# Kernel optimization log

Measured on AMD Instinct MI355X. Metric: run time of the kernel, lower is better.

The kernel has to match this reference:

```python
import jax, jax.numpy as jnp
import numpy as np

ALPHA, BETA, GAMMA = 1.0, 1.0, 0.7
WIN = 11
C1 = 0.01 ** 2
C2 = 0.03 ** 2


def get_sobel_kernels(n1=1, n2=2, n3=2):
    a = np.asarray
    Sx = a([[[-n1, 0, n1], [-n2, 0, n2], [-n1, 0, n1]],
            [[-n2, 0, n2], [-n3 * n2, 0, n3 * n2], [-n2, 0, n2]],
            [[-n1, 0, n1], [-n2, 0, n2], [-n1, 0, n1]]])
    Sy = a([[[-n1, -n2, -n1], [0, 0, 0], [n1, n2, n1]],
            [[-n2, -n3 * n2, -n2], [0, 0, 0], [n2, n3 * n2, n2]],
            [[-n1, -n2, -n1], [0, 0, 0], [n1, n2, n1]]])
    Sz = a([[[-n1, -n2, -n1], [-n2, -n3 * n2, -n2], [-n1, -n2, -n1]],
            [[0, 0, 0], [0, 0, 0], [0, 0, 0]],
            [[n1, n2, n1], [n2, n3 * n2, n2], [n1, n2, n1]]])
    Sd11 = a([[[0, n1, n2], [-n1, 0, n1], [-n2, -n1, 0]],
              [[0, n2, n2 * n3], [-n2, 0, n2], [-n2 * n3, -n2, 0]],
              [[0, n1, n2], [-n1, 0, n1], [-n2, -n1, 0]]])
    Sd12 = a([[[-n2, -n1, 0], [-n1, 0, n1], [0, n1, n2]],
              [[-n2 * n3, -n2, 0], [-n2, 0, n2], [0, n2, n2 * n3]],
              [[-n2, -n1, 0], [-n1, 0, n1], [0, n1, n2]]])
    Sd21 = Sd11.T
    Sd22 = Sd12.T
    Sd31 = a([-S.T for S in Sd11.T])
    Sd32 = a([S.T for S in Sd12.T])
    return np.stack([Sx, Sy, Sz, Sd11, Sd12, Sd21, Sd22, Sd31, Sd32]).astype(np.float32)

# (9,1,3,3,3) fused sobel bank -- single grouped conv instead of 9 launches
SOBEL_W = jnp.asarray(get_sobel_kernels()[:, None])


def _gauss1d():
    g = jnp.exp(-(jnp.arange(WIN, dtype=jnp.float32) - WIN // 2) ** 2 / (2 * 1.5 ** 2))
    return g / g.sum()

G1D = _gauss1d()


def conv3d(x, w):
    return jax.lax.conv_general_dilated(
        x, w, window_strides=(1, 1, 1), padding='SAME',
        dimension_numbers=('NCDHW', 'OIDHW', 'NCDHW'))


def gauss_filter(x):
    # separable 11-tap gaussian along D, H, W (== full 11^3 window, zero-padded SAME)
    x = conv3d(x, G1D.reshape(1, 1, WIN, 1, 1))
    x = conv3d(x, G1D.reshape(1, 1, 1, WIN, 1))
    x = conv3d(x, G1D.reshape(1, 1, 1, 1, WIN))
    return x


def edge_map(img):
    # GradEdge3D.__call__ with a=1, C=1
    B, C, D, H, W = img.shape
    xp = jnp.pad(img, ((0, 0), (0, 0), (1, 1), (1, 1), (1, 1)), mode='reflect')
    g = conv3d(xp, SOBEL_W)                       # (B, 9, D+2, H+2, W+2)
    gm = jnp.sqrt(jnp.sum((g + 1e-6) ** 2 + 1e-6, axis=1))  # (B, D+2, H+2, W+2)
    gm = gm[:, 1:-1, 1:-1, 1:-1]
    norm = (gm - gm.min()) / (gm.max() - gm.min() + 1e-6)
    return norm.reshape(B, 1, D, H, W)


def ssim_value(pred, target):
    mu_p = gauss_filter(pred)
    mu_t = gauss_filter(target)
    mu_p2, mu_t2, mu_pt = mu_p ** 2, mu_t ** 2, mu_p * mu_t
    sig_p = gauss_filter(pred * pred) - mu_p2
    sig_t = gauss_filter(target * target) - mu_t2
    sig_pt = gauss_filter(pred * target) - mu_pt
    ssim_map = ((2 * mu_pt + C1) * (2 * sig_pt + C2)) / ((mu_p2 + mu_t2 + C1) * (sig_p + sig_t + C2))
    return 1.0 - ssim_map.mean()


def setup_inputs() -> dict:
    key = jax.random.key(0)
    k1, k2 = jax.random.split(key)
    shape = (2, 1, 128, 128, 128)
    return {
        'pred': jax.random.uniform(k1, shape, dtype=jnp.float32),
        'target': jax.random.uniform(k2, shape, dtype=jnp.float32),
    }


def reference(pred, target):
    loss_mse = jnp.mean((pred - target) ** 2)
    loss_ssim = ssim_value(pred, target)
    # GMELoss3D: lam_errors=[(1.0, L1Loss())], reduction='sum'
    loss_gme = 1e-6 + jnp.mean(jnp.abs(edge_map(pred) - edge_map(target)))
    total = ALPHA * loss_mse + BETA * loss_ssim + GAMMA * loss_gme
    return (total, loss_mse, loss_ssim, loss_gme)
```

## Files before the change

kernel.cpp:

```cpp
#include <hip/hip_runtime.h>


#define VOL 4194304
#define HV  2097152

typedef _Float16 h2 __attribute__((ext_vector_type(2)));
typedef _Float16 h8 __attribute__((ext_vector_type(8)));

constexpr float GW[11] = {
    0.00102838f, 0.00759876f, 0.03600077f, 0.10936070f, 0.21300554f,
    0.26601173f,
    0.21300554f, 0.10936070f, 0.03600077f, 0.00759876f, 0.00102838f};


__global__ __launch_bounds__(256) void k_init(double* dbl, unsigned int* ui) {
  const int tid = threadIdx.x + (blockIdx.x << 8);
  if (tid < 1536) dbl[tid] = 0.0;
  if (tid < 4096) ui[tid] = (tid < 2048) ? 0x7F800000u : 0u;
}

__device__ __forceinline__ void wblur_body(
    const float* __restrict__ p, const float* __restrict__ t,
    _Float16* __restrict__ A, double* __restrict__ mseB, const int bidx) {
  __shared__ float pr[2][138];
  __shared__ float tr[2][138];
  __shared__ float redw[256];
  const int tid = threadIdx.x;
  const int rl = tid >> 7;
  const int x  = tid & 127;
  const int rowBase = bidx << 4;
  if (x < 5)    { pr[rl][x] = 0.f;      tr[rl][x] = 0.f; }
  if (x >= 123) { pr[rl][10 + x] = 0.f; tr[rl][10 + x] = 0.f; }
  float pv = p[((rowBase + rl) << 7) + x];
  float tv = t[((rowBase + rl) << 7) + x];
  float msel = 0.f;
  for (int it = 0; it < 8; ++it) {
    const int row  = rowBase + (it << 1) + rl;
    const int base = row << 7;
    pr[rl][5 + x] = pv; tr[rl][5 + x] = tv;
    __syncthreads();
    float pvN = 0.f, tvN = 0.f;
    if (it < 7) {
      const int baseN = (row + 2) << 7;
      pvN = p[baseN + x]; tvN = t[baseN + x];
    }
    float ap = 0.f, at = 0.f, app = 0.f, att = 0.f, apt = 0.f;
#pragma unroll
    for (int k = 0; k < 11; ++k) {
      const float w = GW[k];
      const float a = pr[rl][x + k];
      const float b = tr[rl][x + k];
      ap += w * a; at += w * b;
      app += w * a * a; att += w * b * b; apt += w * a * b;
    }
    const int idx = base + x;
    A[idx]           = (_Float16)ap;
    A[VOL + idx]     = (_Float16)at;
    A[2 * VOL + idx] = (_Float16)app;
    A[3 * VOL + idx] = (_Float16)att;
    A[4 * VOL + idx] = (_Float16)apt;
    const float d = pv - tv;
    msel += d * d;
    __syncthreads();
    pv = pvN; tv = tvN;
  }
  redw[tid] = msel;
  __syncthreads();
  for (int s = 128; s > 0; s >>= 1) {
    if (tid < s) redw[tid] += redw[tid + s];
    __syncthreads();
  }
  if (tid == 0) atomicAdd(&mseB[(bidx & 63) << 3], (double)redw[0]);
}

__device__ __forceinline__ void sobel_body(
    const float* __restrict__ p, const float* __restrict__ t,
    _Float16* __restrict__ gmP, _Float16* __restrict__ gmT,
    unsigned int* __restrict__ ui, const int bx, const int by, const int bz) {
  __shared__ float sb[972];
  __shared__ float rmin[256];
  __shared__ float rmax[256];
  const int tid = threadIdx.x;
  const int tx = tid & 15;
  const int ty = tid >> 4;
  const int x0 = bx << 4;
  const int y0 = by << 4;
  const int vol = bz >> 3;
  const int b   = (bz >> 2) & 1;
  const int z0  = (bz & 3) << 5;
  const float* __restrict__ img = vol ? t : p;
  _Float16* __restrict__ gm = vol ? gmT : gmP;
  const int vb = b << 21;

  const int l1 = tid;
  const int ly1 = l1 / 18, lx1 = l1 % 18;
  int gy1 = y0 - 1 + ly1; gy1 = gy1 < 0 ? 1 : (gy1 > 127 ? 126 : gy1);
  int gx1 = x0 - 1 + lx1; gx1 = gx1 < 0 ? 1 : (gx1 > 127 ? 126 : gx1);
  const int off1 = (gy1 << 7) + gx1;
  const int l2 = tid + 256;
  const int ly2 = l2 / 18, lx2 = l2 % 18;
  int gy2 = y0 - 1 + ly2; gy2 = gy2 < 0 ? 1 : (gy2 > 127 ? 126 : gy2);
  int gx2 = x0 - 1 + lx2; gx2 = gx2 < 0 ? 1 : (gx2 > 127 ? 126 : gx2);
  const int off2 = (gy2 << 7) + gx2;
  const bool has2 = (tid < 68);
  const int rb = ty * 18 + tx;
  const int gbase = vb + (z0 << 14) + ((y0 + ty) << 7) + (x0 + tx);

  float Y0[7], Y1[7], Y2[7];
  float rv1 = 0.f, rv2 = 0.f;
  float lmin = 3.4e38f, lmax = 0.f;

#define LOADR(ZS) {                                                         \
    const int zc_ = (ZS) > 127 ? 126 : (ZS);                                \
    const int za_ = vb + (zc_ << 14);                                       \
    rv1 = img[za_ + off1];                                                  \
    if (has2) rv2 = img[za_ + off2]; }

#define WRITELDS(BOFF) {                                                    \
    sb[(BOFF) + l1] = rv1;                                                  \
    if (has2) sb[(BOFF) + l2] = rv2; }

#define COMPY(P) {                                                          \
    const int o_ = (P) * 324 + rb;                                          \
    const float r00 = sb[o_],      r01 = sb[o_ + 1],  r02 = sb[o_ + 2];     \
    const float r10 = sb[o_ + 18], r11 = sb[o_ + 19], r12 = sb[o_ + 20];    \
    const float r20 = sb[o_ + 36], r21 = sb[o_ + 37], r22 = sb[o_ + 38];    \
    const float dx0 = r02 - r00, dx1 = r12 - r10, dx2 = r22 - r20;          \
    const float ux0 = r00 + r01 + r02, ux1 = r10 + r11 + r12,               \
                ux2 = r20 + r21 + r22;                                      \
    const float sx0 = ux0 + r01, sx1 = ux1 + r11, sx2 = ux2 + r21;          \
    Y##P[1] = dx0 + dx1 + dx2;                                    \
    Y##P[0] = Y##P[1] + dx1;                                      \
    Y##P[2] = sx2 - sx0;                                          \
    Y##P[4] = sx0 + sx1 + sx2;                                    \
    Y##P[3] = Y##P[4] + sx1;                                      \
    Y##P[5] = ux2 - ux0;                                          \
    Y##P[6] = (ux0 + ux2) + 2.f * ux1; }

#define EMIT(I, P0, P1, P2) {                                               \
    const float E_ = Y##P0[0] + Y##P1[0] + Y##P2[0];                        \
    const float g1 = E_ + Y##P1[0];                                         \
    const float tA = Y##P0[1] + Y##P1[1] + Y##P2[1];                        \
    const float A_ = tA + Y##P1[1];                                         \
    const float D_ = Y##P0[2] + Y##P1[2] + Y##P2[2];                        \
    const float g2 = D_ + Y##P1[2];                                         \
    const float g3 = Y##P2[3] - Y##P0[3];                                   \
    const float C_ = Y##P2[4] - Y##P0[4];                                   \
    const float B_ = (Y##P0[5] + Y##P2[5]) + 2.f * Y##P1[5];                \
    const float F_ = Y##P2[6] - Y##P0[6];                                   \
    const float g4 = A_ - B_, g5 = A_ + B_;                                 \
    const float g6 = C_ - D_, g7 = C_ + D_;                                 \
    const float g8 = E_ - F_, g9 = E_ + F_;                                 \
    float ss_ = 9e-6f, t_;                                                  \
    t_ = g1 + 1e-6f; ss_ = fmaf(t_, t_, ss_);                               \
    t_ = g2 + 1e-6f; ss_ = fmaf(t_, t_, ss_);                               \
    t_ = g3 + 1e-6f; ss_ = fmaf(t_, t_, ss_);                               \
    t_ = g4 + 1e-6f; ss_ = fmaf(t_, t_, ss_);                               \
    t_ = g5 + 1e-6f; ss_ = fmaf(t_, t_, ss_);                               \
    t_ = g6 + 1e-6f; ss_ = fmaf(t_, t_, ss_);                               \
    t_ = g7 + 1e-6f; ss_ = fmaf(t_, t_, ss_);                               \
    t_ = g8 + 1e-6f; ss_ = fmaf(t_, t_, ss_);                               \
    t_ = g9 + 1e-6f; ss_ = fmaf(t_, t_, ss_);                               \
    const _Float16 gh = (_Float16)sqrtf(ss_);                               \
    gm[gbase + ((I) << 14)] = gh;                                           \
    const float gq = (float)gh;                                             \
    lmin = fminf(lmin, gq); lmax = fmaxf(lmax, gq); }

#define BODY(I, P0, P1, P2) {                                               \
    WRITELDS((P2) * 324);                                                   \
    LOADR(z0 + (I) + 2);                                                    \
    __syncthreads();                                                        \
    COMPY(P2);                                                              \
    EMIT(I, P0, P1, P2); }

  {
    const int zp = (z0 == 0) ? 1 : (z0 - 1);
    LOADR(zp);  WRITELDS(0);
    LOADR(z0);  WRITELDS(324);
    __syncthreads();
    COMPY(0);
    COMPY(1);
    LOADR(z0 + 1);
  }
  for (int ii = 0; ii < 30; ii += 3) {
    BODY(ii,     0, 1, 2);
    BODY(ii + 1, 1, 2, 0);
    BODY(ii + 2, 2, 0, 1);
  }
  BODY(30, 0, 1, 2);
  BODY(31, 1, 2, 0);

#undef BODY
#undef EMIT
#undef COMPY
#undef WRITELDS
#undef LOADR

  rmin[tid] = lmin; rmax[tid] = lmax;
  __syncthreads();
  for (int st = 128; st > 0; st >>= 1) {
    if (tid < st) {
      rmin[tid] = fminf(rmin[tid], rmin[tid + st]);
      rmax[tid] = fmaxf(rmax[tid], rmax[tid + st]);
    }
    __syncthreads();
  }
  if (tid == 0) {
    const int bin = (bx + (by << 3) + (bz << 6)) & 63;
    atomicMin(&ui[vol * 1024 + (bin << 4)], __float_as_uint(rmin[0]));
    atomicMax(&ui[2048 + vol * 1024 + (bin << 4)], __float_as_uint(rmax[0]));
  }
}

__device__ __forceinline__ void blury_body(
    const _Float16* __restrict__ A, _Float16* __restrict__ B,
    const int z, const int yseg, const int batch) {
  __shared__ h8 s[5][26][16];
  const int tid = threadIdx.x;
  const int y0 = yseg << 4;
  const int b8 = batch << 18;
  const h8* __restrict__ Ah = (const h8*)A;
  h8* __restrict__ Bh = (h8*)B;
  const int slice8 = b8 + (z << 11);
  for (int q = 0; q < 5; ++q) {
    const h8* __restrict__ Aq = Ah + (q << 19) + slice8;
    for (int l = tid; l < 416; l += 256) {
      const int row = l >> 4, xc = l & 15;
      const int y = y0 - 5 + row;
      h8 v{};
      if ((unsigned)y < 128u) v = Aq[(y << 4) + xc];
      s[q][row][xc] = v;
    }
  }
  __syncthreads();
  const int xc = tid & 15;
  const int yo = tid >> 4;
  const int wbase = slice8 + ((y0 + yo) << 4) + xc;
#pragma unroll
  for (int q = 0; q < 5; ++q) {
    h8 acc{};
#pragma unroll
    for (int k = 0; k < 11; ++k) {
      const _Float16 w = (_Float16)GW[k];
      acc += w * s[q][yo + k][xc];
    }
    Bh[(q << 19) + wbase] = acc;
  }
}

__device__ __forceinline__ void edge_body(
    const _Float16* __restrict__ gmP, const _Float16* __restrict__ gmT,
    const unsigned int* __restrict__ ui, double* __restrict__ absB,
    const int bidx) {
  __shared__ float rede[256];
  float mnp = 3.4e38f, mnt = 3.4e38f, mxp = 0.f, mxt = 0.f;
  for (int j = 0; j < 64; ++j) {
    mnp = fminf(mnp, __uint_as_float(ui[j << 4]));
    mnt = fminf(mnt, __uint_as_float(ui[1024 + (j << 4)]));
    mxp = fmaxf(mxp, __uint_as_float(ui[2048 + (j << 4)]));
    mxt = fmaxf(mxt, __uint_as_float(ui[3072 + (j << 4)]));
  }
  const float scp = 1.f / (mxp - mnp + 1e-6f);
  const float sct = 1.f / (mxt - mnt + 1e-6f);
  const h8* __restrict__ gp = (const h8*)gmP;
  const h8* __restrict__ gt = (const h8*)gmT;
  float lsum = 0.f;
  const int base = bidx << 9;
#pragma unroll
  for (int i = 0; i < 2; ++i) {
    const int idx = base + (i << 8) + threadIdx.x;
    const h8 a = gp[idx];
    const h8 b = gt[idx];
#pragma unroll
    for (int j = 0; j < 8; ++j)
      lsum += fabsf(((float)a[j] - mnp) * scp - ((float)b[j] - mnt) * sct);
  }
  rede[threadIdx.x] = lsum;
  __syncthreads();
  for (int s = 128; s > 0; s >>= 1) {
    if (threadIdx.x < s) rede[threadIdx.x] += rede[threadIdx.x + s];
    __syncthreads();
  }
  if (threadIdx.x == 0)
    atomicAdd(&absB[(bidx & 63) << 3], (double)rede[0]);
}

__global__ __launch_bounds__(256) void k_fused_a(
    const float* __restrict__ p, const float* __restrict__ t,
    _Float16* __restrict__ A, double* __restrict__ mseB,
    _Float16* __restrict__ gmP, _Float16* __restrict__ gmT,
    unsigned int* __restrict__ ui) {
  const int bid = blockIdx.x;
  const int r3 = bid % 3;
  if (r3 < 2) {
    wblur_body(p, t, A, mseB, (bid / 3) * 2 + r3);
  } else {
    const int s = bid / 3;
    sobel_body(p, t, gmP, gmT, ui, s & 7, (s >> 3) & 7, s >> 6);
  }
}

__global__ __launch_bounds__(256) void k_fused_b(
    const _Float16* __restrict__ A, _Float16* __restrict__ B,
    const _Float16* __restrict__ gmP, const _Float16* __restrict__ gmT,
    const unsigned int* __restrict__ ui, double* __restrict__ absB) {
  const int bid = blockIdx.x;
  const int r3 = bid % 3;
  if (r3 < 2) {
    const int idx = (bid / 3) * 2 + r3;
    blury_body(A, B, idx & 127, (idx >> 7) & 7, idx >> 10);
  } else {
    edge_body(gmP, gmT, ui, absB, bid / 3);
  }
}

__global__ __launch_bounds__(256) void k_zblur_ssim(
    const _Float16* __restrict__ B, double* __restrict__ ssimB) {
  __shared__ h8 s[5][26][16];
  __shared__ float red[256];
  const int tid = threadIdx.x;
  const int y  = blockIdx.x;
  const int z0 = blockIdx.y << 4;
  const int b8 = blockIdx.z << 18;
  const h8* __restrict__ Bh = (const h8*)B;
  const int col8 = b8 + (y << 4);
  for (int q = 0; q < 5; ++q) {
    const h8* __restrict__ Bq = Bh + (q << 19) + col8;
    for (int l = tid; l < 416; l += 256) {
      const int row = l >> 4, xc = l & 15;
      const int zz = z0 - 5 + row;
      h8 v{};
      if ((unsigned)zz < 128u) v = Bq[(zz << 11) + xc];
      s[q][row][xc] = v;
    }
  }
  __syncthreads();
  const int xc = tid & 15;
  const int zo = tid >> 4;
  h8 m[5];
#pragma unroll
  for (int q = 0; q < 5; ++q) {
    h8 acc{};
#pragma unroll
    for (int k = 0; k < 11; ++k) {
      const _Float16 w = (_Float16)GW[k];
      acc += w * s[q][zo + k][xc];
    }
    m[q] = acc;
  }
  float lsum = 0.f;
#pragma unroll
  for (int j = 0; j < 8; ++j) {
    const float mp  = (float)m[0][j];
    const float mt  = (float)m[1][j];
    const float epp = (float)m[2][j];
    const float ett = (float)m[3][j];
    const float ept = (float)m[4][j];
    const float mp2 = mp * mp, mt2 = mt * mt, mpt = mp * mt;
    const float num = (2.f * mpt + 1e-4f) * (2.f * (ept - mpt) + 9e-4f);
    const float den = (mp2 + mt2 + 1e-4f) * ((epp - mp2) + (ett - mt2) + 9e-4f);
    lsum += num / den;
  }
  red[tid] = lsum;
  __syncthreads();
  for (int st = 128; st > 0; st >>= 1) {
    if (tid < st) red[tid] += red[tid + st];
    __syncthreads();
  }
  if (tid == 0) {
    const int bin = (blockIdx.x + (blockIdx.y << 3) + blockIdx.z) & 63;
    atomicAdd(&ssimB[bin << 3], (double)red[0]);
  }
}

__global__ void k_final(const double* __restrict__ dbl, float* __restrict__ out) {
  if (threadIdx.x == 0 && blockIdx.x == 0) {
    double ms = 0.0, ss = 0.0, ab = 0.0;
    for (int j = 0; j < 64; ++j) {
      ms += dbl[j << 3];
      ss += dbl[512 + (j << 3)];
      ab += dbl[1024 + (j << 3)];
    }
    const double N = 4194304.0;
    const double mse   = ms / N;
    const double ssiml = 1.0 - ss / N;
    const double gme   = 1e-6 + ab / N;
    const double total = mse + ssiml + 0.7 * gme;
    out[0] = (float)total;
    out[1] = (float)mse;
    out[2] = (float)ssiml;
    out[3] = (float)gme;
  }
}

extern "C" void kernel_launch(void* const* d_in, const int* in_sizes, int n_in,
                              void* d_out, int out_size, void* d_ws, size_t ws_size,
                              hipStream_t stream) {
  const float* p = (const float*)d_in[0];
  const float* t = (const float*)d_in[1];
  _Float16* A = (_Float16*)d_ws;
  _Float16* B = A + (size_t)5 * VOL;
  char* accb = (char*)d_ws + (size_t)20 * VOL;
  double* dbl = (double*)accb;
  unsigned int* ui = (unsigned int*)(accb + 12288);
  _Float16* gmP = (_Float16*)((char*)d_ws + 88080384);
  _Float16* gmT = gmP + VOL;
  float* out = (float*)d_out;

  k_init<<<16, 256, 0, stream>>>(dbl, ui);
  k_fused_a<<<3072, 256, 0, stream>>>(p, t, A, dbl, gmP, gmT, ui);
  k_fused_b<<<3072, 256, 0, stream>>>(A, B, gmP, gmT, ui, dbl + 1024);
  k_zblur_ssim<<<dim3(128, 8, 2), 256, 0, stream>>>(B, dbl + 512);
  k_final<<<1, 64, 0, stream>>>(dbl, out);
}
```

Measured before the change: 161.6 us.

## Blur sum/difference fields to cut SSIM channels from five to four

SSIM statistics are rebuilt from blurs of s=p+t and d=p-t and their squares instead of p, t, p², t², pt. This cuts the blurred fp16 channels from five to four, reducing memory traffic and arithmetic in all three blur passes. Separately, the Sobel LDS tile row stride is padded from 18 to 24 floats, likely to change bank mapping. The algebraic rewrite subtracts nearly equal fp16 quantities, so cancellation can cost some precision in the variance terms.

```diff
diff --git a/kernel.cpp b/kernel.cpp
--- a/kernel.cpp
+++ b/kernel.cpp
@@ -22,45 +22,47 @@
 __device__ __forceinline__ void wblur_body(
     const float* __restrict__ p, const float* __restrict__ t,
     _Float16* __restrict__ A, double* __restrict__ mseB, const int bidx) {
-  __shared__ float pr[2][138];
-  __shared__ float tr[2][138];
+  __shared__ float sr[2][138];
+  __shared__ float dr[2][138];
   __shared__ float redw[256];
   const int tid = threadIdx.x;
   const int rl = tid >> 7;
   const int x  = tid & 127;
   const int rowBase = bidx << 4;
-  if (x < 5)    { pr[rl][x] = 0.f;      tr[rl][x] = 0.f; }
-  if (x >= 123) { pr[rl][10 + x] = 0.f; tr[rl][10 + x] = 0.f; }
+  if (x < 5)    { sr[rl][x] = 0.f;      dr[rl][x] = 0.f; }
+  if (x >= 123) { sr[rl][10 + x] = 0.f; dr[rl][10 + x] = 0.f; }
   float pv = p[((rowBase + rl) << 7) + x];
   float tv = t[((rowBase + rl) << 7) + x];
   float msel = 0.f;
   for (int it = 0; it < 8; ++it) {
     const int row  = rowBase + (it << 1) + rl;
     const int base = row << 7;
-    pr[rl][5 + x] = pv; tr[rl][5 + x] = tv;
+    const float sv = pv + tv;
+    const float dv = pv - tv;
+    sr[rl][5 + x] = sv; dr[rl][5 + x] = dv;
+    msel += dv * dv;
     __syncthreads();
     float pvN = 0.f, tvN = 0.f;
     if (it < 7) {
       const int baseN = (row + 2) << 7;
       pvN = p[baseN + x]; tvN = t[baseN + x];
     }
-    float ap = 0.f, at = 0.f, app = 0.f, att = 0.f, apt = 0.f;
+    float as = 0.f, ad = 0.f, ass = 0.f, add_ = 0.f;
 #pragma unroll
     for (int k = 0; k < 11; ++k) {
       const float w = GW[k];
-      const float a = pr[rl][x + k];
-      const float b = tr[rl][x + k];
-      ap += w * a; at += w * b;
-      app += w * a * a; att += w * b * b; apt += w * a * b;
+      const float a = sr[rl][x + k];
+      const float b = dr[rl][x + k];
+      const float wa = w * a;
+      const float wb = w * b;
+      as += wa; ad += wb;
+      ass += wa * a; add_ += wb * b;
     }
     const int idx = base + x;
-    A[idx]           = (_Float16)ap;
-    A[VOL + idx]     = (_Float16)at;
-    A[2 * VOL + idx] = (_Float16)app;
-    A[3 * VOL + idx] = (_Float16)att;
-    A[4 * VOL + idx] = (_Float16)apt;
-    const float d = pv - tv;
-    msel += d * d;
+    A[idx]           = (_Float16)as;
+    A[VOL + idx]     = (_Float16)ad;
+    A[2 * VOL + idx] = (_Float16)ass;
+    A[3 * VOL + idx] = (_Float16)add_;
     __syncthreads();
     pv = pvN; tv = tvN;
   }
@@ -77,7 +79,7 @@
     const float* __restrict__ p, const float* __restrict__ t,
     _Float16* __restrict__ gmP, _Float16* __restrict__ gmT,
     unsigned int* __restrict__ ui, const int bx, const int by, const int bz) {
-  __shared__ float sb[972];
+  __shared__ float sb[1296];
   __shared__ float rmin[256];
   __shared__ float rmax[256];
   const int tid = threadIdx.x;
@@ -94,16 +96,18 @@
 
   const int l1 = tid;
   const int ly1 = l1 / 18, lx1 = l1 % 18;
+  const int la1 = ly1 * 24 + lx1;
   int gy1 = y0 - 1 + ly1; gy1 = gy1 < 0 ? 1 : (gy1 > 127 ? 126 : gy1);
   int gx1 = x0 - 1 + lx1; gx1 = gx1 < 0 ? 1 : (gx1 > 127 ? 126 : gx1);
   const int off1 = (gy1 << 7) + gx1;
   const int l2 = tid + 256;
   const int ly2 = l2 / 18, lx2 = l2 % 18;
+  const int la2 = ly2 * 24 + lx2;
   int gy2 = y0 - 1 + ly2; gy2 = gy2 < 0 ? 1 : (gy2 > 127 ? 126 : gy2);
   int gx2 = x0 - 1 + lx2; gx2 = gx2 < 0 ? 1 : (gx2 > 127 ? 126 : gx2);
   const int off2 = (gy2 << 7) + gx2;
   const bool has2 = (tid < 68);
-  const int rb = ty * 18 + tx;
+  const int rb = ty * 24 + tx;
   const int gbase = vb + (z0 << 14) + ((y0 + ty) << 7) + (x0 + tx);
 
   float Y0[7], Y1[7], Y2[7];
@@ -117,14 +121,14 @@
     if (has2) rv2 = img[za_ + off2]; }
 
 #define WRITELDS(BOFF) {                                                    \
-    sb[(BOFF) + l1] = rv1;                                                  \
-    if (has2) sb[(BOFF) + l2] = rv2; }
+    sb[(BOFF) + la1] = rv1;                                                 \
+    if (has2) sb[(BOFF) + la2] = rv2; }
 
 #define COMPY(P) {                                                          \
-    const int o_ = (P) * 324 + rb;                                          \
+    const int o_ = (P) * 432 + rb;                                          \
     const float r00 = sb[o_],      r01 = sb[o_ + 1],  r02 = sb[o_ + 2];     \
-    const float r10 = sb[o_ + 18], r11 = sb[o_ + 19], r12 = sb[o_ + 20];    \
-    const float r20 = sb[o_ + 36], r21 = sb[o_ + 37], r22 = sb[o_ + 38];    \
+    const float r10 = sb[o_ + 24], r11 = sb[o_ + 25], r12 = sb[o_ + 26];    \
+    const float r20 = sb[o_ + 48], r21 = sb[o_ + 49], r22 = sb[o_ + 50];    \
     const float dx0 = r02 - r00, dx1 = r12 - r10, dx2 = r22 - r20;          \
     const float ux0 = r00 + r01 + r02, ux1 = r10 + r11 + r12,               \
                 ux2 = r20 + r21 + r22;                                      \
@@ -167,7 +171,7 @@
     lmin = fminf(lmin, gq); lmax = fmaxf(lmax, gq); }
 
 #define BODY(I, P0, P1, P2) {                                               \
-    WRITELDS((P2) * 324);                                                   \
+    WRITELDS((P2) * 432);                                                   \
     LOADR(z0 + (I) + 2);                                                    \
     __syncthreads();                                                        \
     COMPY(P2);                                                              \
@@ -176,7 +180,7 @@
   {
     const int zp = (z0 == 0) ? 1 : (z0 - 1);
     LOADR(zp);  WRITELDS(0);
-    LOADR(z0);  WRITELDS(324);
+    LOADR(z0);  WRITELDS(432);
     __syncthreads();
     COMPY(0);
     COMPY(1);
@@ -215,14 +219,14 @@
 __device__ __forceinline__ void blury_body(
     const _Float16* __restrict__ A, _Float16* __restrict__ B,
     const int z, const int yseg, const int batch) {
-  __shared__ h8 s[5][26][16];
+  __shared__ h8 s[4][26][16];
   const int tid = threadIdx.x;
   const int y0 = yseg << 4;
   const int b8 = batch << 18;
   const h8* __restrict__ Ah = (const h8*)A;
   h8* __restrict__ Bh = (h8*)B;
   const int slice8 = b8 + (z << 11);
-  for (int q = 0; q < 5; ++q) {
+  for (int q = 0; q < 4; ++q) {
     const h8* __restrict__ Aq = Ah + (q << 19) + slice8;
     for (int l = tid; l < 416; l += 256) {
       const int row = l >> 4, xc = l & 15;
@@ -237,7 +241,7 @@
   const int yo = tid >> 4;
   const int wbase = slice8 + ((y0 + yo) << 4) + xc;
 #pragma unroll
-  for (int q = 0; q < 5; ++q) {
+  for (int q = 0; q < 4; ++q) {
     h8 acc{};
 #pragma unroll
     for (int k = 0; k < 11; ++k) {
@@ -316,7 +320,7 @@
 
 __global__ __launch_bounds__(256) void k_zblur_ssim(
     const _Float16* __restrict__ B, double* __restrict__ ssimB) {
-  __shared__ h8 s[5][26][16];
+  __shared__ h8 s[4][26][16];
   __shared__ float red[256];
   const int tid = threadIdx.x;
   const int y  = blockIdx.x;
@@ -324,7 +328,7 @@
   const int b8 = blockIdx.z << 18;
   const h8* __restrict__ Bh = (const h8*)B;
   const int col8 = b8 + (y << 4);
-  for (int q = 0; q < 5; ++q) {
+  for (int q = 0; q < 4; ++q) {
     const h8* __restrict__ Bq = Bh + (q << 19) + col8;
     for (int l = tid; l < 416; l += 256) {
       const int row = l >> 4, xc = l & 15;
@@ -337,9 +341,9 @@
   __syncthreads();
   const int xc = tid & 15;
   const int zo = tid >> 4;
-  h8 m[5];
-#pragma unroll
-  for (int q = 0; q < 5; ++q) {
+  h8 m[4];
+#pragma unroll
+  for (int q = 0; q < 4; ++q) {
     h8 acc{};
 #pragma unroll
     for (int k = 0; k < 11; ++k) {
@@ -351,14 +355,15 @@
   float lsum = 0.f;
 #pragma unroll
   for (int j = 0; j < 8; ++j) {
-    const float mp  = (float)m[0][j];
-    const float mt  = (float)m[1][j];
-    const float epp = (float)m[2][j];
-    const float ett = (float)m[3][j];
-    const float ept = (float)m[4][j];
-    const float mp2 = mp * mp, mt2 = mt * mt, mpt = mp * mt;
-    const float num = (2.f * mpt + 1e-4f) * (2.f * (ept - mpt) + 9e-4f);
-    const float den = (mp2 + mt2 + 1e-4f) * ((epp - mp2) + (ett - mt2) + 9e-4f);
+    const float mus = (float)m[0][j];
+    const float mud = (float)m[1][j];
+    const float ess = (float)m[2][j];
+    const float edd = (float)m[3][j];
+    const float S2 = mus * mus, D2 = mud * mud;
+    const float num = ((S2 - D2) * 0.5f + 1e-4f) *
+                      ((ess - edd - S2 + D2) * 0.5f + 9e-4f);
+    const float den = ((S2 + D2) * 0.5f + 1e-4f) *
+                      ((ess + edd - S2 - D2) * 0.5f + 9e-4f);
     lsum += num / den;
   }
   red[tid] = lsum;
@@ -399,7 +404,7 @@
   const float* p = (const float*)d_in[0];
   const float* t = (const float*)d_in[1];
   _Float16* A = (_Float16*)d_ws;
-  _Float16* B = A + (size_t)5 * VOL;
+  _Float16* B = A + (size_t)4 * VOL;
   char* accb = (char*)d_ws + (size_t)20 * VOL;
   double* dbl = (double*)accb;
   unsigned int* ui = (unsigned int*)(accb + 12288);
```

Result: faster. 150.8 us (-6.7%).
